# Kernel tuning notes

Measured on AMD Instinct MI355X. Metric: run time of the kernel, lower is better.

Reference implementation:

```python
import jax, jax.numpy as jnp
import numpy as np

B, L, S = 32, 128, 96
EMBED, HIDDEN = 768, 300
NUM_POS, NUM_DEP, NUM_REL = 50, 40, 41  # NUM_REL = num_dependencies + 1
NUM_LAYERS, NUM_LABEL = 2, 3


def setup_inputs() -> dict:
    key = jax.random.key(0)
    ks = jax.random.split(key, 12)
    text = jax.random.normal(ks[0], (B, L, EMBED), dtype=jnp.float32)
    context_masks = jnp.ones((B, L), dtype=jnp.int64)
    pos_tags = jax.random.randint(ks[1], (B, S), 0, NUM_POS)
    adjacency_tensors = jax.random.uniform(ks[2], (B, NUM_REL, S, S), dtype=jnp.float32)
    # learned parameters
    pos_emb = jax.random.normal(ks[3], (NUM_POS, EMBED), dtype=jnp.float32) * 0.02
    pos_emb = pos_emb.at[0].set(0.0)  # padding_idx=0
    lin_W = jax.random.normal(ks[4], (EMBED, HIDDEN), dtype=jnp.float32) * 0.02
    lin_b = jnp.zeros((HIDDEN,), dtype=jnp.float32)
    rgcn_W = jax.random.normal(ks[5], (NUM_LAYERS, NUM_REL, HIDDEN, HIDDEN), dtype=jnp.float32) * 0.05
    score_W = jax.random.normal(ks[6], (NUM_LAYERS, HIDDEN), dtype=jnp.float32) * 0.05
    score_b = jnp.zeros((NUM_LAYERS,), dtype=jnp.float32)
    dense_W = jax.random.normal(ks[7], (2 * HIDDEN, NUM_LABEL), dtype=jnp.float32) * 0.02
    dense_b = jnp.zeros((NUM_LABEL,), dtype=jnp.float32)
    return dict(text=text, context_masks=context_masks, pos_tags=pos_tags,
                adjacency_tensors=adjacency_tensors, pos_emb=pos_emb,
                lin_W=lin_W, lin_b=lin_b, rgcn_W=rgcn_W, score_W=score_W,
                score_b=score_b, dense_W=dense_W, dense_b=dense_b)


def rgcn_layer(x, adj, W, sw, sb):
    # x: [B,S,H], adj: [B,R,S,S], W: [R,H,H]
    hidden = jnp.einsum('bsi,rio->brso', x, W)           # per-relation transform
    denom = jnp.sum(adj, axis=3, keepdims=True)          # [B,R,S,1]
    intm = jnp.einsum('brst,brto->brso', adj, hidden)    # adjacency aggregation
    div = intm / jnp.where(denom == 0.0, 1.0, denom)     # safe normalize
    scores = jnp.einsum('brso,o->brs', div, sw) + sb     # relation attention logits
    r = jax.nn.softmax(scores, axis=1)                   # softmax over relations
    out = jnp.einsum('brso,brs->bso', div, r)            # weighted combine
    return jax.nn.relu(out)


def reference(text, context_masks, pos_tags, adjacency_tensors, pos_emb,
              lin_W, lin_b, rgcn_W, score_W, score_b, dense_W, dense_b):
    embedding_len = jnp.sum(context_masks, axis=-1).astype(jnp.float32)  # [B]
    text_out = text @ lin_W + lin_b                                      # embed_dim != hidden_dim path
    hc = text_out                                                        # [B,L,H]
    review_text_len = jnp.sum(pos_tags != 0, axis=-1).astype(jnp.float32)
    review = pos_emb[pos_tags] @ lin_W + lin_b                           # [B,S,H]
    hg = review
    for l in range(NUM_LAYERS):
        hg = rgcn_layer(hg, adjacency_tensors, rgcn_W[l], score_W[l], score_b[l])
    hc_mean = jnp.sum(hc, axis=1) / embedding_len[:, None]
    hg_mean = jnp.sum(hg, axis=1) / review_text_len[:, None]
    final_x = jnp.concatenate([hg_mean, hc_mean], axis=-1)
    return final_x @ dense_W + dense_b                                   # [B, num_label]
```

## Files before the change

### kernel.cpp

```cpp
#include <hip/hip_runtime.h>

#define NB 32
#define NLEN 128
#define NS 96
#define NE 768
#define NH 300
#define NR 41
#define RCH 7
#define RPC 6
#define OCT 5

#define OFF_TSUM   0u
#define OFF_ELEN   24576u
#define OFF_RLEN   24608u
#define OFF_HCM    24640u
#define OFF_TAB    34240u
#define OFF_HGA    49240u
#define OFF_HGB    970840u
#define OFF_SWT    1892440u
#define OFF_U      1904740u
#define OFF_SPRE   2030692u
#define OFF_RDEN   2156644u
#define OFF_C      2282596u
#define OFF_P      2408548u

__device__ __forceinline__ int SW(int o) { return o + ((o >> 5) << 2); }

__device__ __forceinline__ float wave_reduce(float v) {
#pragma unroll
  for (int off = 32; off > 0; off >>= 1) v += __shfl_down(v, off);
  return v;
}

__global__ void k_tsum(const float* __restrict__ text, float* __restrict__ tsum) {
  int b = blockIdx.x;
  int tid = threadIdx.x;
  for (int e = tid; e < NE; e += 256) {
    const float* p = text + (size_t)b * NLEN * NE + e;
    float s = 0.f;
#pragma unroll 4
    for (int l = 0; l < NLEN; ++l) s += p[(size_t)l * NE];
    tsum[b * NE + e] = s;
  }
}

__global__ void k_len(const int* __restrict__ cm, const int* __restrict__ pt,
                      float* __restrict__ elen, float* __restrict__ rlen) {
  int b = threadIdx.x;
  if (b < NB) {
    int s1 = 0;
    for (int l = 0; l < NLEN; ++l) s1 += cm[b * NLEN + l];
    int s2 = 0;
    for (int s = 0; s < NS; ++s) s2 += (pt[b * NS + s] != 0) ? 1 : 0;
    elen[b] = (float)s1;
    rlen[b] = (float)s2;
  }
}

__global__ void k_hcmean(const float* __restrict__ tsum, const float* __restrict__ linW,
                         const float* __restrict__ linb, const float* __restrict__ elen,
                         float* __restrict__ hcm) {
  int idx = blockIdx.x * 256 + threadIdx.x;
  if (idx >= NB * NH) return;
  int b = idx / NH, h = idx - b * NH;
  const float* tp = tsum + b * NE;
  float s = 0.f;
  for (int e = 0; e < NE; ++e) s += tp[e] * linW[(size_t)e * NH + h];
  hcm[idx] = (s + (float)NLEN * linb[h]) / elen[b];
}

__global__ void k_table(const float* __restrict__ pemb, const float* __restrict__ linW,
                        const float* __restrict__ linb, float* __restrict__ tab) {
  int idx = blockIdx.x * 256 + threadIdx.x;
  if (idx >= 50 * NH) return;
  int p = idx / NH, h = idx - p * NH;
  const float* pp = pemb + (size_t)p * NE;
  float s = 0.f;
  for (int e = 0; e < NE; ++e) s += pp[e] * linW[(size_t)e * NH + h];
  tab[idx] = s + linb[h];
}

__global__ void k_gather(const int* __restrict__ pt, const float* __restrict__ tab,
                         float* __restrict__ hg) {
  int idx = blockIdx.x * 256 + threadIdx.x;
  if (idx >= NB * NS * NH) return;
  int h = idx % NH;
  int bs = idx / NH;
  hg[idx] = tab[pt[bs] * NH + h];
}

__global__ void k_swt(const float* __restrict__ Wl, const float* __restrict__ sw,
                      float* __restrict__ swt) {
  int gw = (blockIdx.x * blockDim.x + threadIdx.x) >> 6;
  int lane = threadIdx.x & 63;
  if (gw >= NR * NH) return;
  const float* wp = Wl + (size_t)gw * NH;
  float s = 0.f;
  for (int o = lane; o < NH; o += 64) s += wp[o] * sw[o];
  s = wave_reduce(s);
  if (lane == 0) swt[gw] = s;
}

__global__ void k_u(const float* __restrict__ x, const float* __restrict__ swt,
                    float* __restrict__ u) {
  int gw = (blockIdx.x * blockDim.x + threadIdx.x) >> 6;
  int lane = threadIdx.x & 63;
  if (gw >= NB * NR * NS) return;
  int t = gw % NS;
  int br = gw / NS;
  int r = br % NR;
  int b = br / NR;
  const float* xp = x + (size_t)(b * NS + t) * NH;
  const float* sp = swt + (size_t)r * NH;
  float s = 0.f;
  for (int i = lane; i < NH; i += 64) s += xp[i] * sp[i];
  s = wave_reduce(s);
  if (lane == 0) u[gw] = s;
}

__global__ void k_scores(const float* __restrict__ adj, const float* __restrict__ u,
                         const float* __restrict__ sb, float* __restrict__ spre,
                         float* __restrict__ rden) {
  int gw = (blockIdx.x * blockDim.x + threadIdx.x) >> 6;
  int lane = threadIdx.x & 63;
  if (gw >= NB * NR * NS) return;
  int s = gw % NS;
  int br = gw / NS;
  int r = br % NR;
  int b = br / NR;
  const float* ap = adj + (size_t)gw * NS;
  const float* up = u + (size_t)br * NS;
  float d = 0.f, v = 0.f;
  for (int t = lane; t < NS; t += 64) {
    float a = ap[t];
    d += a;
    v += a * up[t];
  }
  d = wave_reduce(d);
  v = wave_reduce(v);
  if (lane == 0) {
    float ds = (d == 0.f) ? 1.f : d;
    int o = (b * NS + s) * NR + r;
    spre[o] = v / ds + sb[0];
    rden[o] = 1.f / ds;
  }
}

__global__ void k_softmax(const float* __restrict__ spre, const float* __restrict__ rden,
                          float* __restrict__ c) {
  int bs = blockIdx.x * 256 + threadIdx.x;
  if (bs >= NB * NS) return;
  int b = bs / NS, s = bs - b * NS;
  float vals[NR];
  float m = -1e30f;
#pragma unroll
  for (int r = 0; r < NR; ++r) {
    vals[r] = spre[(size_t)bs * NR + r];
    m = fmaxf(m, vals[r]);
  }
  float sum = 0.f;
#pragma unroll
  for (int r = 0; r < NR; ++r) {
    float e = expf(vals[r] - m);
    vals[r] = e;
    sum += e;
  }
  float inv = 1.f / sum;
#pragma unroll
  for (int r = 0; r < NR; ++r) {
    c[((size_t)(b * NR + r)) * NS + s] = vals[r] * inv * rden[(size_t)bs * NR + r];
  }
}

__global__ __launch_bounds__(192)
void k_fused(const float* __restrict__ adj, const float* __restrict__ x,
             const float* __restrict__ cbuf, const float* __restrict__ Wl,
             float* __restrict__ P) {
  __shared__ __align__(16) float sA[32 * 108];
  __shared__ __align__(16) float sB[32 * 68];
  __shared__ __align__(16) float sH[96 * 68];

  const int tid = threadIdx.x;
  int bid = blockIdx.x;
  const int oc = bid % OCT; bid /= OCT;
  const int rg = bid % RCH;
  const int b = bid / RCH;
  const int o0 = oc * 64;
  const int r0 = rg * RPC;
  const int nr = (r0 + RPC <= NR) ? RPC : (NR - r0);

  const int g1 = tid >> 3;
  const int g2 = tid & 7;
  const int fa = SW(g1 * 4);
  const int fb = SW(g2 * 8);

  float accO[4][8];
#pragma unroll
  for (int i = 0; i < 4; ++i)
#pragma unroll
    for (int j = 0; j < 8; ++j) accO[i][j] = 0.f;

  const float* xb = x + (size_t)b * NS * NH;

  for (int rr = 0; rr < nr; ++rr) {
    const int r = r0 + rr;
    const float* wp = Wl + (size_t)r * NH * NH;
    const float* ap = adj + (size_t)(b * NR + r) * NS * NS;
    const float* cp = cbuf + (size_t)(b * NR + r) * NS;

    float acc1[4][8];
#pragma unroll
    for (int i = 0; i < 4; ++i)
#pragma unroll
      for (int j = 0; j < 8; ++j) acc1[i][j] = 0.f;

    for (int kc = 0; kc < 10; ++kc) {
      const int k0 = kc * 32;
      __syncthreads();
#pragma unroll
      for (int p = 0; p < 4; ++p) {
        int idx = tid + p * 192;
        int kq = (idx & 7) * 4;
        int t = idx >> 3;
        int k = k0 + kq;
        float4 v = make_float4(0.f, 0.f, 0.f, 0.f);
        if (k + 3 < NH) v = *(const float4*)&xb[t * NH + k];
        int col = SW(t);
        sA[(kq + 0) * 108 + col] = v.x;
        sA[(kq + 1) * 108 + col] = v.y;
        sA[(kq + 2) * 108 + col] = v.z;
        sA[(kq + 3) * 108 + col] = v.w;
      }
#pragma unroll
      for (int p = 0; p < 3; ++p) {
        int idx = tid + p * 192;
        if (idx < 512) {
          int oq = (idx & 15) * 4;
          int kk = idx >> 4;
          int k = k0 + kk;
          int o = o0 + oq;
          float4 v = make_float4(0.f, 0.f, 0.f, 0.f);
          if (k < NH) {
            const float* wrow = wp + (size_t)k * NH;
            v.x = (o + 0 < NH) ? wrow[o + 0] : 0.f;
            v.y = (o + 1 < NH) ? wrow[o + 1] : 0.f;
            v.z = (o + 2 < NH) ? wrow[o + 2] : 0.f;
            v.w = (o + 3 < NH) ? wrow[o + 3] : 0.f;
          }
          *(float4*)&sB[kk * 68 + SW(oq)] = v;
        }
      }
      __syncthreads();
#pragma unroll
      for (int kk = 0; kk < 32; ++kk) {
        float4 a = *(const float4*)&sA[kk * 108 + fa];
        float4 b0 = *(const float4*)&sB[kk * 68 + fb];
        float4 b1 = *(const float4*)&sB[kk * 68 + fb + 4];
        float as[4] = {a.x, a.y, a.z, a.w};
        float bs[8] = {b0.x, b0.y, b0.z, b0.w, b1.x, b1.y, b1.z, b1.w};
#pragma unroll
        for (int i = 0; i < 4; ++i)
#pragma unroll
          for (int j = 0; j < 8; ++j) acc1[i][j] += as[i] * bs[j];
      }
    }

#pragma unroll
    for (int i = 0; i < 4; ++i) {
      float4 h0 = make_float4(acc1[i][0], acc1[i][1], acc1[i][2], acc1[i][3]);
      float4 h1 = make_float4(acc1[i][4], acc1[i][5], acc1[i][6], acc1[i][7]);
      *(float4*)&sH[(g1 * 4 + i) * 68 + fb] = h0;
      *(float4*)&sH[(g1 * 4 + i) * 68 + fb + 4] = h1;
    }

    for (int tc = 0; tc < 3; ++tc) {
      const int t0 = tc * 32;
      __syncthreads();
#pragma unroll
      for (int p = 0; p < 4; ++p) {
        int idx = tid + p * 192;
        int tq = (idx & 7) * 4;
        int s = idx >> 3;
        float4 v = *(const float4*)&ap[s * NS + t0 + tq];
        float cs = cp[s];
        int col = SW(s);
        sA[(tq + 0) * 108 + col] = v.x * cs;
        sA[(tq + 1) * 108 + col] = v.y * cs;
        sA[(tq + 2) * 108 + col] = v.z * cs;
        sA[(tq + 3) * 108 + col] = v.w * cs;
      }
      __syncthreads();
#pragma unroll
      for (int kk = 0; kk < 32; ++kk) {
        float4 a = *(const float4*)&sA[kk * 108 + fa];
        float4 b0 = *(const float4*)&sH[(t0 + kk) * 68 + fb];
        float4 b1 = *(const float4*)&sH[(t0 + kk) * 68 + fb + 4];
        float as[4] = {a.x, a.y, a.z, a.w};
        float bs[8] = {b0.x, b0.y, b0.z, b0.w, b1.x, b1.y, b1.z, b1.w};
#pragma unroll
        for (int i = 0; i < 4; ++i)
#pragma unroll
          for (int j = 0; j < 8; ++j) accO[i][j] += as[i] * bs[j];
      }
    }
  }

  float* pp = P + ((size_t)rg * NB + b) * NS * NH;
#pragma unroll
  for (int i = 0; i < 4; ++i) {
    int s = g1 * 4 + i;
    int o = o0 + g2 * 8;
    float* row = pp + (size_t)s * NH + o;
    if (o + 7 < NH) {
      *(float4*)&row[0] = make_float4(accO[i][0], accO[i][1], accO[i][2], accO[i][3]);
      *(float4*)&row[4] = make_float4(accO[i][4], accO[i][5], accO[i][6], accO[i][7]);
    } else {
#pragma unroll
      for (int j = 0; j < 8; ++j)
        if (o + j < NH) row[j] = accO[i][j];
    }
  }
}

__global__ void k_reduce(const float* __restrict__ P, float* __restrict__ y) {
  int idx = blockIdx.x * 256 + threadIdx.x;
  if (idx >= NB * NS * NH) return;
  float s = 0.f;
#pragma unroll
  for (int ch = 0; ch < RCH; ++ch) s += P[(size_t)ch * (NB * NS * NH) + idx];
  y[idx] = fmaxf(s, 0.f);
}

__global__ void k_final(const float* __restrict__ hg, const float* __restrict__ rlen,
                        const float* __restrict__ hcm, const float* __restrict__ dW,
                        const float* __restrict__ db, float* __restrict__ out) {
  int b = blockIdx.x;
  __shared__ float hgm[NH];
  int tid = threadIdx.x;
  for (int h = tid; h < NH; h += 256) {
    float s = 0.f;
    for (int ss = 0; ss < NS; ++ss) s += hg[((size_t)(b * NS) + ss) * NH + h];
    hgm[h] = s / rlen[b];
  }
  __syncthreads();
  if (tid < 3) {
    float s = db[tid];
    for (int h = 0; h < NH; ++h) s += hgm[h] * dW[h * 3 + tid];
    for (int h = 0; h < NH; ++h) s += hcm[b * NH + h] * dW[(NH + h) * 3 + tid];
    out[b * 3 + tid] = s;
  }
}

extern "C" void kernel_launch(void* const* d_in, const int* in_sizes, int n_in,
                              void* d_out, int out_size, void* d_ws, size_t ws_size,
                              hipStream_t stream) {
  (void)in_sizes; (void)n_in; (void)out_size; (void)ws_size;
  const float* text   = (const float*)d_in[0];
  const int*   cmask  = (const int*)d_in[1];
  const int*   ptags  = (const int*)d_in[2];
  const float* adj    = (const float*)d_in[3];
  const float* pemb   = (const float*)d_in[4];
  const float* linW   = (const float*)d_in[5];
  const float* linb   = (const float*)d_in[6];
  const float* rgcnW  = (const float*)d_in[7];
  const float* scoreW = (const float*)d_in[8];
  const float* scoreB = (const float*)d_in[9];
  const float* denseW = (const float*)d_in[10];
  const float* denseB = (const float*)d_in[11];
  float* out = (float*)d_out;
  float* ws = (float*)d_ws;

  float* tsum = ws + OFF_TSUM;
  float* elen = ws + OFF_ELEN;
  float* rlen = ws + OFF_RLEN;
  float* hcm  = ws + OFF_HCM;
  float* tab  = ws + OFF_TAB;
  float* hgA  = ws + OFF_HGA;
  float* hgB  = ws + OFF_HGB;
  float* swt  = ws + OFF_SWT;
  float* ubuf = ws + OFF_U;
  float* spre = ws + OFF_SPRE;
  float* rden = ws + OFF_RDEN;
  float* cbuf = ws + OFF_C;
  float* Pbuf = ws + OFF_P;

  k_tsum<<<dim3(NB), dim3(256), 0, stream>>>(text, tsum);
  k_len<<<dim3(1), dim3(64), 0, stream>>>(cmask, ptags, elen, rlen);
  k_hcmean<<<dim3((NB * NH + 255) / 256), dim3(256), 0, stream>>>(tsum, linW, linb, elen, hcm);
  k_table<<<dim3((50 * NH + 255) / 256), dim3(256), 0, stream>>>(pemb, linW, linb, tab);
  k_gather<<<dim3((NB * NS * NH + 255) / 256), dim3(256), 0, stream>>>(ptags, tab, hgA);

  float* x = hgA;
  float* yb = hgB;
  for (int l = 0; l < 2; ++l) {
    const float* Wl = rgcnW + (size_t)l * NR * NH * NH;
    k_swt<<<dim3((NR * NH) / 4), dim3(256), 0, stream>>>(Wl, scoreW + l * NH, swt);
    k_u<<<dim3((NB * NR * NS) / 4), dim3(256), 0, stream>>>(x, swt, ubuf);
    k_scores<<<dim3((NB * NR * NS) / 4), dim3(256), 0, stream>>>(adj, ubuf, scoreB + l, spre, rden);
    k_softmax<<<dim3((NB * NS + 255) / 256), dim3(256), 0, stream>>>(spre, rden, cbuf);
    k_fused<<<dim3(NB * RCH * OCT), dim3(192), 0, stream>>>(adj, x, cbuf, Wl, Pbuf);
    k_reduce<<<dim3((NB * NS * NH + 255) / 256), dim3(256), 0, stream>>>(Pbuf, yb);
    float* tswap = x; x = yb; yb = tswap;
  }
  k_final<<<dim3(NB), dim3(256), 0, stream>>>(x, rlen, hcm, denseW, denseB, out);
}
```

Baseline: 2.087 ms.

## Software-pipeline global loads in fused RGCN kernel and regroup relation chunks

Restructures the fused RGCN kernel's inner loops into one flattened 13-step-per-relation loop. The global loads for the next step (x, W, or adjacency tiles) are prefetched into registers while the current shared-memory tile is computed, hiding global-memory latency. W loads become vectorized float4. Relations are split into 5 chunks (9,8,8,8,8) instead of 7 chunks of 6, with a remapped block index for scheduling, which also cuts the partial-sum buffer reduced later. Extra prefetch registers may lower occupancy, and the grid now has fewer blocks.

New measurement: 2.589 ms. +24.1%, slower.

```diff
diff --git a/kernel.cpp b/kernel.cpp
--- a/kernel.cpp
+++ b/kernel.cpp
@@ -6,8 +6,7 @@
 #define NE 768
 #define NH 300
 #define NR 41
-#define RCH 7
-#define RPC 6
+#define RCH 5
 #define OCT 5
 
 #define OFF_TSUM   0u
@@ -181,76 +180,132 @@
   __shared__ __align__(16) float sH[96 * 68];
 
   const int tid = threadIdx.x;
-  int bid = blockIdx.x;
-  const int oc = bid % OCT; bid /= OCT;
-  const int rg = bid % RCH;
-  const int b = bid / RCH;
+  int w = ((blockIdx.x & 7) * 100) + (blockIdx.x >> 3);
+  const int oc = w % 5; w /= 5;
+  const int rg = w % 5;
+  const int b = w / 5;
   const int o0 = oc * 64;
-  const int r0 = rg * RPC;
-  const int nr = (r0 + RPC <= NR) ? RPC : (NR - r0);
+  const int r0 = (rg == 0) ? 0 : (9 + (rg - 1) * 8);
+  const int nr = (rg == 0) ? 9 : 8;
+
+  const int arow = tid >> 3;
+  const int akq  = (tid & 7) * 4;
+  const int wo4  = (tid & 15) * 4;
+  const int wk   = tid >> 4;
+  const int wsw  = SW(wo4);
+  const bool wv2 = (tid < 128);
+  const bool wov = (o0 + wo4 + 4 <= NH);
 
   const int g1 = tid >> 3;
   const int g2 = tid & 7;
   const int fa = SW(g1 * 4);
   const int fb = SW(g2 * 8);
 
+  const float* xb = x + (size_t)b * NS * NH;
+
   float accO[4][8];
 #pragma unroll
   for (int i = 0; i < 4; ++i)
 #pragma unroll
     for (int j = 0; j < 8; ++j) accO[i][j] = 0.f;
-
-  const float* xb = x + (size_t)b * NS * NH;
-
-  for (int rr = 0; rr < nr; ++rr) {
-    const int r = r0 + rr;
-    const float* wp = Wl + (size_t)r * NH * NH;
-    const float* ap = adj + (size_t)(b * NR + r) * NS * NS;
-    const float* cp = cbuf + (size_t)(b * NR + r) * NS;
-
-    float acc1[4][8];
-#pragma unroll
-    for (int i = 0; i < 4; ++i)
-#pragma unroll
-      for (int j = 0; j < 8; ++j) acc1[i][j] = 0.f;
-
-    for (int kc = 0; kc < 10; ++kc) {
-      const int k0 = kc * 32;
-      __syncthreads();
-#pragma unroll
-      for (int p = 0; p < 4; ++p) {
-        int idx = tid + p * 192;
-        int kq = (idx & 7) * 4;
-        int t = idx >> 3;
-        int k = k0 + kq;
-        float4 v = make_float4(0.f, 0.f, 0.f, 0.f);
-        if (k + 3 < NH) v = *(const float4*)&xb[t * NH + k];
-        int col = SW(t);
-        sA[(kq + 0) * 108 + col] = v.x;
-        sA[(kq + 1) * 108 + col] = v.y;
-        sA[(kq + 2) * 108 + col] = v.z;
-        sA[(kq + 3) * 108 + col] = v.w;
+  float acc1[4][8];
+
+  float4 pa0, pa1, pa2, pa3;
+  float4 pw0, pw1, pw2;
+  float pc0, pc1, pc2, pc3;
+
+  const float4 fz = make_float4(0.f, 0.f, 0.f, 0.f);
+
+#define ISSUE(RR, IT)                                                          \
+  do {                                                                         \
+    const int r_ = r0 + (RR);                                                  \
+    if ((IT) < 10) {                                                           \
+      const int k0_ = (IT) * 32;                                               \
+      const int kx_ = k0_ + akq;                                               \
+      if (kx_ + 4 <= NH) {                                                     \
+        pa0 = *(const float4*)&xb[(arow +  0) * NH + kx_];                     \
+        pa1 = *(const float4*)&xb[(arow + 24) * NH + kx_];                     \
+        pa2 = *(const float4*)&xb[(arow + 48) * NH + kx_];                     \
+        pa3 = *(const float4*)&xb[(arow + 72) * NH + kx_];                     \
+      } else { pa0 = fz; pa1 = fz; pa2 = fz; pa3 = fz; }                       \
+      const float* wp_ = Wl + (size_t)r_ * NH * NH;                            \
+      const int ow_ = o0 + wo4;                                                \
+      const int kw0_ = k0_ + wk;                                               \
+      pw0 = (wov && kw0_ < NH) ? *(const float4*)&wp_[(size_t)kw0_ * NH + ow_] : fz; \
+      const int kw1_ = kw0_ + 12;                                              \
+      pw1 = (wov && kw1_ < NH) ? *(const float4*)&wp_[(size_t)kw1_ * NH + ow_] : fz; \
+      const int kw2_ = kw0_ + 24;                                              \
+      pw2 = (wv2 && wov && kw2_ < NH) ? *(const float4*)&wp_[(size_t)kw2_ * NH + ow_] : fz; \
+    } else {                                                                   \
+      const int t0_ = ((IT) - 10) * 32;                                        \
+      const float* ap_ = adj + (size_t)(b * NR + r_) * NS * NS;                \
+      const float* cp_ = cbuf + (size_t)(b * NR + r_) * NS;                    \
+      pa0 = *(const float4*)&ap_[(arow +  0) * NS + t0_ + akq];                \
+      pa1 = *(const float4*)&ap_[(arow + 24) * NS + t0_ + akq];                \
+      pa2 = *(const float4*)&ap_[(arow + 48) * NS + t0_ + akq];                \
+      pa3 = *(const float4*)&ap_[(arow + 72) * NS + t0_ + akq];                \
+      pc0 = cp_[arow]; pc1 = cp_[arow + 24];                                   \
+      pc2 = cp_[arow + 48]; pc3 = cp_[arow + 72];                              \
+    }                                                                          \
+  } while (0)
+
+  ISSUE(0, 0);
+
+  int rr = 0, it = 0;
+  const int tot = nr * 13;
+  for (int s = 0; s < tot; ++s) {
+    __syncthreads();
+
+    if (it == 10) {
+#pragma unroll
+      for (int i = 0; i < 4; ++i) {
+        *(float4*)&sH[(g1 * 4 + i) * 68 + fb] =
+            make_float4(acc1[i][0], acc1[i][1], acc1[i][2], acc1[i][3]);
+        *(float4*)&sH[(g1 * 4 + i) * 68 + fb + 4] =
+            make_float4(acc1[i][4], acc1[i][5], acc1[i][6], acc1[i][7]);
       }
-#pragma unroll
-      for (int p = 0; p < 3; ++p) {
-        int idx = tid + p * 192;
-        if (idx < 512) {
-          int oq = (idx & 15) * 4;
-          int kk = idx >> 4;
-          int k = k0 + kk;
-          int o = o0 + oq;
-          float4 v = make_float4(0.f, 0.f, 0.f, 0.f);
-          if (k < NH) {
-            const float* wrow = wp + (size_t)k * NH;
-            v.x = (o + 0 < NH) ? wrow[o + 0] : 0.f;
-            v.y = (o + 1 < NH) ? wrow[o + 1] : 0.f;
-            v.z = (o + 2 < NH) ? wrow[o + 2] : 0.f;
-            v.w = (o + 3 < NH) ? wrow[o + 3] : 0.f;
-          }
-          *(float4*)&sB[kk * 68 + SW(oq)] = v;
-        }
+    }
+
+    if (it < 10) {
+      const int c0 = SW(arow), c1 = SW(arow + 24), c2 = SW(arow + 48), c3 = SW(arow + 72);
+      sA[(akq + 0) * 108 + c0] = pa0.x; sA[(akq + 1) * 108 + c0] = pa0.y;
+      sA[(akq + 2) * 108 + c0] = pa0.z; sA[(akq + 3) * 108 + c0] = pa0.w;
+      sA[(akq + 0) * 108 + c1] = pa1.x; sA[(akq + 1) * 108 + c1] = pa1.y;
+      sA[(akq + 2) * 108 + c1] = pa1.z; sA[(akq + 3) * 108 + c1] = pa1.w;
+      sA[(akq + 0) * 108 + c2] = pa2.x; sA[(akq + 1) * 108 + c2] = pa2.y;
+      sA[(akq + 2) * 108 + c2] = pa2.z; sA[(akq + 3) * 108 + c2] = pa2.w;
+      sA[(akq + 0) * 108 + c3] = pa3.x; sA[(akq + 1) * 108 + c3] = pa3.y;
+      sA[(akq + 2) * 108 + c3] = pa3.z; sA[(akq + 3) * 108 + c3] = pa3.w;
+      *(float4*)&sB[(wk + 0) * 68 + wsw] = pw0;
+      *(float4*)&sB[(wk + 12) * 68 + wsw] = pw1;
+      if (wv2) *(float4*)&sB[(wk + 24) * 68 + wsw] = pw2;
+    } else {
+      const int c0 = SW(arow), c1 = SW(arow + 24), c2 = SW(arow + 48), c3 = SW(arow + 72);
+      sA[(akq + 0) * 108 + c0] = pa0.x * pc0; sA[(akq + 1) * 108 + c0] = pa0.y * pc0;
+      sA[(akq + 2) * 108 + c0] = pa0.z * pc0; sA[(akq + 3) * 108 + c0] = pa0.w * pc0;
+      sA[(akq + 0) * 108 + c1] = pa1.x * pc1; sA[(akq + 1) * 108 + c1] = pa1.y * pc1;
+      sA[(akq + 2) * 108 + c1] = pa1.z * pc1; sA[(akq + 3) * 108 + c1] = pa1.w * pc1;
+      sA[(akq + 0) * 108 + c2] = pa2.x * pc2; sA[(akq + 1) * 108 + c2] = pa2.y * pc2;
+      sA[(akq + 2) * 108 + c2] = pa2.z * pc2; sA[(akq + 3) * 108 + c2] = pa2.w * pc2;
+      sA[(akq + 0) * 108 + c3] = pa3.x * pc3; sA[(akq + 1) * 108 + c3] = pa3.y * pc3;
+      sA[(akq + 2) * 108 + c3] = pa3.z * pc3; sA[(akq + 3) * 108 + c3] = pa3.w * pc3;
+    }
+
+    if (s + 1 < tot) {
+      int it2 = it + 1, rr2 = rr;
+      if (it2 == 13) { it2 = 0; ++rr2; }
+      ISSUE(rr2, it2);
+    }
+
+    __syncthreads();
+
+    if (it < 10) {
+      if (it == 0) {
+#pragma unroll
+        for (int i = 0; i < 4; ++i)
+#pragma unroll
+          for (int j = 0; j < 8; ++j) acc1[i][j] = 0.f;
       }
-      __syncthreads();
 #pragma unroll
       for (int kk = 0; kk < 32; ++kk) {
         float4 a = *(const float4*)&sA[kk * 108 + fa];
@@ -263,33 +318,8 @@
 #pragma unroll
           for (int j = 0; j < 8; ++j) acc1[i][j] += as[i] * bs[j];
       }
-    }
-
-#pragma unroll
-    for (int i = 0; i < 4; ++i) {
-      float4 h0 = make_float4(acc1[i][0], acc1[i][1], acc1[i][2], acc1[i][3]);
-      float4 h1 = make_float4(acc1[i][4], acc1[i][5], acc1[i][6], acc1[i][7]);
-      *(float4*)&sH[(g1 * 4 + i) * 68 + fb] = h0;
-      *(float4*)&sH[(g1 * 4 + i) * 68 + fb + 4] = h1;
-    }
-
-    for (int tc = 0; tc < 3; ++tc) {
-      const int t0 = tc * 32;
-      __syncthreads();
-#pragma unroll
-      for (int p = 0; p < 4; ++p) {
-        int idx = tid + p * 192;
-        int tq = (idx & 7) * 4;
-        int s = idx >> 3;
-        float4 v = *(const float4*)&ap[s * NS + t0 + tq];
-        float cs = cp[s];
-        int col = SW(s);
-        sA[(tq + 0) * 108 + col] = v.x * cs;
-        sA[(tq + 1) * 108 + col] = v.y * cs;
-        sA[(tq + 2) * 108 + col] = v.z * cs;
-        sA[(tq + 3) * 108 + col] = v.w * cs;
-      }
-      __syncthreads();
+    } else {
+      const int t0 = (it - 10) * 32;
 #pragma unroll
       for (int kk = 0; kk < 32; ++kk) {
         float4 a = *(const float4*)&sA[kk * 108 + fa];
@@ -303,14 +333,18 @@
           for (int j = 0; j < 8; ++j) accO[i][j] += as[i] * bs[j];
       }
     }
-  }
+
+    ++it;
+    if (it == 13) { it = 0; ++rr; }
+  }
+#undef ISSUE
 
   float* pp = P + ((size_t)rg * NB + b) * NS * NH;
 #pragma unroll
   for (int i = 0; i < 4; ++i) {
-    int s = g1 * 4 + i;
+    int srow = g1 * 4 + i;
     int o = o0 + g2 * 8;
-    float* row = pp + (size_t)s * NH + o;
+    float* row = pp + (size_t)srow * NH + o;
     if (o + 7 < NH) {
       *(float4*)&row[0] = make_float4(accO[i][0], accO[i][1], accO[i][2], accO[i][3]);
       *(float4*)&row[4] = make_float4(accO[i][4], accO[i][5], accO[i][6], accO[i][7]);
```

## Alias shared buffers, rebalance relation chunks, swizzle block order for occupancy

Applied to the files above, without the earlier changes.

The sB and sH shared buffers now share one allocation, and the H tile is written after the first barrier of the aggregation loop. This cuts LDS per block so three blocks can fit per CU, a target the launch-bounds hint also states. Relations are split into 5 chunks (9,8,8,8,8) instead of 7 chunks of 6, which reduces partial-sum traffic in the reduce step but gives each block more serial work. The block index is also remapped with an interleaved swizzle, likely to spread batches across XCDs for cache locality.

New measurement: 2.434 ms. +16.6%, slower.

```diff
diff --git a/kernel.cpp b/kernel.cpp
--- a/kernel.cpp
+++ b/kernel.cpp
@@ -6,8 +6,7 @@
 #define NE 768
 #define NH 300
 #define NR 41
-#define RCH 7
-#define RPC 6
+#define RCH 5
 #define OCT 5
 
 #define OFF_TSUM   0u
@@ -172,22 +171,23 @@
   }
 }
 
-__global__ __launch_bounds__(192)
+__global__ __launch_bounds__(192, 3)
 void k_fused(const float* __restrict__ adj, const float* __restrict__ x,
              const float* __restrict__ cbuf, const float* __restrict__ Wl,
              float* __restrict__ P) {
-  __shared__ __align__(16) float sA[32 * 108];
-  __shared__ __align__(16) float sB[32 * 68];
-  __shared__ __align__(16) float sH[96 * 68];
+  __shared__ __align__(16) float smem[9984];
+  float* sA = smem;
+  float* sB = smem + 3456;
+  float* sH = smem + 3456;
 
   const int tid = threadIdx.x;
-  int bid = blockIdx.x;
-  const int oc = bid % OCT; bid /= OCT;
-  const int rg = bid % RCH;
-  const int b = bid / RCH;
+  int w = ((blockIdx.x & 7) * 100) + (blockIdx.x >> 3);
+  const int oc = w % 5; w /= 5;
+  const int rg = w % 5;
+  const int b = w / 5;
   const int o0 = oc * 64;
-  const int r0 = rg * RPC;
-  const int nr = (r0 + RPC <= NR) ? RPC : (NR - r0);
+  const int r0 = (rg == 0) ? 0 : (9 + (rg - 1) * 8);
+  const int nr = (rg == 0) ? 9 : 8;
 
   const int g1 = tid >> 3;
   const int g2 = tid & 7;
@@ -265,17 +265,18 @@
       }
     }
 
-#pragma unroll
-    for (int i = 0; i < 4; ++i) {
-      float4 h0 = make_float4(acc1[i][0], acc1[i][1], acc1[i][2], acc1[i][3]);
-      float4 h1 = make_float4(acc1[i][4], acc1[i][5], acc1[i][6], acc1[i][7]);
-      *(float4*)&sH[(g1 * 4 + i) * 68 + fb] = h0;
-      *(float4*)&sH[(g1 * 4 + i) * 68 + fb + 4] = h1;
-    }
-
     for (int tc = 0; tc < 3; ++tc) {
       const int t0 = tc * 32;
       __syncthreads();
+      if (tc == 0) {
+#pragma unroll
+        for (int i = 0; i < 4; ++i) {
+          *(float4*)&sH[(g1 * 4 + i) * 68 + fb] =
+              make_float4(acc1[i][0], acc1[i][1], acc1[i][2], acc1[i][3]);
+          *(float4*)&sH[(g1 * 4 + i) * 68 + fb + 4] =
+              make_float4(acc1[i][4], acc1[i][5], acc1[i][6], acc1[i][7]);
+        }
+      }
 #pragma unroll
       for (int p = 0; p < 4; ++p) {
         int idx = tid + p * 192;
@@ -308,9 +309,9 @@
   float* pp = P + ((size_t)rg * NB + b) * NS * NH;
 #pragma unroll
   for (int i = 0; i < 4; ++i) {
-    int s = g1 * 4 + i;
+    int srow = g1 * 4 + i;
     int o = o0 + g2 * 8;
-    float* row = pp + (size_t)s * NH + o;
+    float* row = pp + (size_t)srow * NH + o;
     if (o + 7 < NH) {
       *(float4*)&row[0] = make_float4(accO[i][0], accO[i][1], accO[i][2], accO[i][3]);
       *(float4*)&row[4] = make_float4(accO[i][4], accO[i][5], accO[i][6], accO[i][7]);
```
